# Kernel optimization log

Hardware: AMD Instinct MI355X
Metric: run time of the kernel (lower is better)

## Reference

```python
import jax, jax.numpy as jnp
import numpy as np

B, NAV, H, W = 16, 36, 120, 160
HID, AEMB, NF = 512, 32, 4

def _conv(x, w, b, stride, pad, dil, groups):
    y = jax.lax.conv_general_dilated(x, w, stride, pad, rhs_dilation=dil, feature_group_count=groups)
    return y + b[None, :, None, None]

def _avgpool(x, k, s):
    y = jax.lax.reduce_window(x, 0.0, jax.lax.add, (1, 1) + k, (1, 1) + s, 'VALID')
    return y / float(k[0] * k[1])

def _conv2_block(x, w1, b1, w2, b2):
    # conv2_1: k5 stride (5,7) dilation 10 -> avgpool 3/3 -> conv2_2: k3 stride 2 dilation (1,2) -> avgpool (3,9)/3
    y = _conv(x, w1, b1, (5, 7), ((0, 0), (0, 0)), (10, 10), 1)
    y = _avgpool(y, (3, 3), (3, 3))
    y = _conv(y, w2, b2, (2, 2), ((0, 0), (0, 0)), (1, 2), 1)
    y = _avgpool(y, (3, 9), (3, 3))
    return y[:, 0]  # [B,3,12]

def setup_inputs() -> dict:
    key = jax.random.key(0)
    ks = jax.random.split(key, 24)
    s = 0.02
    d = {}
    d['depth_feat_0'] = jax.random.normal(ks[0], (B, NAV, H, W), jnp.float32)
    d['depth_feat_1'] = jax.random.normal(ks[1], (B, NAV, H, W), jnp.float32)
    d['obj_detection_feat'] = jax.random.normal(ks[2], (B, NAV, H, W), jnp.float32)
    d['num_navigable_feat'] = jax.random.uniform(ks[3], (B, NAV), jnp.float32)
    d['pre_action_feat'] = jax.random.normal(ks[4], (B, AEMB), jnp.float32)
    d['h_0'] = jax.random.normal(ks[5], (B, HID), jnp.float32)
    d['c_0'] = jax.random.normal(ks[6], (B, HID), jnp.float32)
    d['weighted_ctx'] = jax.random.normal(ks[7], (B, HID), jnp.float32)
    d['navigable_index'] = jax.random.randint(ks[8], (B, 8), 0, NAV).astype(jnp.int32)
    # params
    d['conv1_w'] = jax.random.normal(ks[9], (NAV, 2, 5, 5), jnp.float32) * s
    d['conv1_b'] = jnp.zeros((NAV,), jnp.float32)
    d['dyn_filters'] = jax.random.normal(ks[10], (NF, NAV, 2, 5, 5), jnp.float32) * s
    d['dyn_w1'] = jax.random.normal(ks[11], (HID, HID // 4), jnp.float32) * s
    d['dyn_b1'] = jnp.zeros((HID // 4,), jnp.float32)
    d['dyn_w2'] = jax.random.normal(ks[12], (HID // 4, NF), jnp.float32) * s
    d['dyn_b2'] = jnp.zeros((NF,), jnp.float32)
    d['conv2_1_w'] = jax.random.normal(ks[13], (1, 1, 5, 5), jnp.float32) * s
    d['conv2_1_b'] = jnp.zeros((1,), jnp.float32)
    d['conv2_2_w'] = jax.random.normal(ks[14], (1, 1, 3, 3), jnp.float32) * s
    d['conv2_2_b'] = jnp.zeros((1,), jnp.float32)
    in_sz = HID + NAV + NF + AEMB  # 584
    d['lstm_w_ih'] = jax.random.normal(ks[15], (4 * HID, in_sz), jnp.float32) * s
    d['lstm_w_hh'] = jax.random.normal(ks[16], (4 * HID, HID), jnp.float32) * s
    d['lstm_b_ih'] = jnp.zeros((4 * HID,), jnp.float32)
    d['lstm_b_hh'] = jnp.zeros((4 * HID,), jnp.float32)
    return d

def reference(depth_feat_0, depth_feat_1, obj_detection_feat, num_navigable_feat, pre_action_feat, h_0, c_0, weighted_ctx, navigable_index, conv1_w, conv1_b, dyn_filters, dyn_w1, dyn_b1, dyn_w2, dyn_b2, conv2_1_w, conv2_1_b, conv2_2_w, conv2_2_b, lstm_w_ih, lstm_w_hh, lstm_b_ih, lstm_b_hh):
    Bv = depth_feat_0.shape[0]
    # interleave depth channels: [B,72,H,W] (replaces 36-iter python copy loop)
    mid1 = jnp.stack([depth_feat_0, depth_feat_1], axis=2).reshape(Bv, 2 * NAV, H, W)
    total_depth = _conv(mid1, conv1_w, conv1_b, (1, 1), ((2, 2), (2, 2)), (1, 1), NAV)  # [B,36,H,W]
    nav_attn = jax.nn.softmax(num_navigable_feat, axis=1)[:, :, None, None]
    mid2 = jnp.stack([total_depth * nav_attn, obj_detection_feat * nav_attn], axis=2).reshape(Bv, 2 * NAV, H, W)
    # dynamic conv: per-sample filter = attention-weighted mix of NF learned grouped filters
    filt_attn = jax.nn.softmax(jax.nn.relu(weighted_ctx @ dyn_w1 + dyn_b1) @ dyn_w2 + dyn_b2, axis=1)  # [B,4]
    kern = jnp.einsum('bf,fgikl->bgikl', filt_attn, dyn_filters).reshape(Bv * NAV, 2, 5, 5)
    dyn_out = jax.lax.conv_general_dilated(mid2.reshape(1, Bv * 2 * NAV, H, W), kern, (1, 1), ((2, 2), (2, 2)), feature_group_count=Bv * NAV).reshape(Bv, NAV, H, W)
    # panorama canvas assembly: tile i -> row block (2 - i//12), col i%12
    canvas = dyn_out.reshape(Bv, 3, 12, H, W)[:, ::-1].transpose(0, 1, 3, 2, 4).reshape(Bv, 1, 3 * H, 12 * W)
    v1 = _conv2_block(canvas, conv2_1_w, conv2_1_b, conv2_2_w, conv2_2_b)
    rolled = jnp.concatenate([canvas[..., -W:], canvas[..., :-W]], axis=-1)
    v2 = _conv2_block(rolled, conv2_1_w, conv2_1_b, conv2_2_w, conv2_2_b)
    v2 = jnp.concatenate([v2[:, :, 1:], v2[:, :, :1]], axis=-1)
    vf = ((v1 + v2) * 0.5)[:, ::-1].reshape(Bv, NAV)  # flip row dim then flatten
    vf = jax.nn.softmax(vf / 10.0, axis=1)  # self.softmax_temperature hardcoded to 10
    concat = jnp.concatenate([weighted_ctx, vf, filt_attn, pre_action_feat], axis=1)
    gates = concat @ lstm_w_ih.T + lstm_b_ih + h_0 @ lstm_w_hh.T + lstm_b_hh
    i, f, g, o = jnp.split(gates, 4, axis=1)
    c_1 = jax.nn.sigmoid(f) * c_0 + jax.nn.sigmoid(i) * jnp.tanh(g)
    h_1 = jax.nn.sigmoid(o) * jnp.tanh(c_1)
    mask = jnp.zeros((Bv, NAV + 1), jnp.float32).at[:, 0].set(1.0)
    mask = mask.at[jnp.arange(Bv)[:, None], navigable_index + 1].set(1.0)
    return (h_1, c_1, vf, mask)
```

## Files before the change

kernel.cpp:

```cpp
#include <hip/hip_runtime.h>
#include <math.h>

#define B_ 16
#define NAV_ 36
#define H_ 120
#define W_ 160
#define HID_ 512
#define PLANES (B_*NAV_)
#define PLANE_PX (H_*W_)
#define CANVAS_H 360
#define CANVAS_W 1920
#define CANVAS_PX (CANVAS_H*CANVAS_W)

#define OUT_H 12
#define IN_ROWS 20
#define TD_ROWS 16
#define OBJ_ROWS 16
#define ROWB 352
#define INCH (IN_ROWS*ROWB)
#define NSLOT (2*IN_ROWS*44 + OBJ_ROWS*44)
#define SPT 10

#define WS_NAV    0
#define WS_FATT   576
#define WS_KERN   640
#define WS_TD     29440
#define WS_CANVAS (WS_TD + PLANES*PLANE_PX)
#define WS_POOL1  (WS_CANVAS + B_*CANVAS_PX)
#define WS_VF     (WS_POOL1 + B_*2*19*89)

typedef unsigned int u32;
typedef _Float16 h2_t __attribute__((ext_vector_type(2)));
typedef float float4a __attribute__((ext_vector_type(4), aligned(4)));

__device__ __forceinline__ float sigmoidf_(float x) { return 1.f / (1.f + expf(-x)); }

__device__ __forceinline__ u32 pkh(float a, float b) {
    return __builtin_bit_cast(u32, __builtin_amdgcn_cvt_pkrtz(a, b));
}
__device__ __forceinline__ float dot2h(u32 a, u32 b, float c) {
#if __has_builtin(__builtin_amdgcn_fdot2)
    return __builtin_amdgcn_fdot2(__builtin_bit_cast(h2_t, a),
                                  __builtin_bit_cast(h2_t, b), c, false);
#else
    float r;
    asm("v_dot2_f32_f16 %0, %1, %2, %3" : "=v"(r) : "v"(a), "v"(b), "v"(c));
    return r;
#endif
}

__device__ __forceinline__ void conv8(const unsigned char* b0, const unsigned char* b1,
                                      const u32* ew, float* acc)
{
    #pragma unroll
    for (int ky = 0; ky < 5; ++ky) {
        const int off = ky*ROWB;
        int4 qa = *(const int4*)(b0 + off);
        int2 qb = *(const int2*)(b0 + off + 16);
        int4 ra = *(const int4*)(b1 + off);
        int2 rb = *(const int2*)(b1 + off + 16);
        u32 P[6] = {(u32)qa.x,(u32)qa.y,(u32)qa.z,(u32)qa.w,(u32)qb.x,(u32)qb.y};
        u32 Q[6] = {(u32)ra.x,(u32)ra.y,(u32)ra.z,(u32)ra.w,(u32)rb.x,(u32)rb.y};
        const u32 e0 = ew[ky*3+0], e1 = ew[ky*3+1], e2 = ew[ky*3+2];
        const u32 f0 = ew[15+ky*3+0], f1 = ew[15+ky*3+1], f2 = ew[15+ky*3+2];
        const u32 o0 = e0 << 16;
        const u32 o1 = __builtin_amdgcn_alignbit(e1, e0, 16);
        const u32 o2 = __builtin_amdgcn_alignbit(e2, e1, 16);
        const u32 g0 = f0 << 16;
        const u32 g1 = __builtin_amdgcn_alignbit(f1, f0, 16);
        const u32 g2 = __builtin_amdgcn_alignbit(f2, f1, 16);
        #pragma unroll
        for (int m = 0; m < 4; ++m) {
            acc[2*m]   = dot2h(e0, P[m], dot2h(e1, P[m+1], dot2h(e2, P[m+2], acc[2*m])));
            acc[2*m+1] = dot2h(o0, P[m], dot2h(o1, P[m+1], dot2h(o2, P[m+2], acc[2*m+1])));
            acc[2*m]   = dot2h(f0, Q[m], dot2h(f1, Q[m+1], dot2h(f2, Q[m+2], acc[2*m])));
            acc[2*m+1] = dot2h(g0, Q[m], dot2h(g1, Q[m+1], dot2h(g2, Q[m+2], acc[2*m+1])));
        }
    }
}

#define LOAD_EW(EW, SW)                                                        \
    {                                                                          \
        _Pragma("unroll")                                                      \
        for (int q = 0; q < 7; ++q) {                                          \
            int4 t_ = ((const int4*)(SW))[q];                                  \
            EW[4*q]=(u32)t_.x; EW[4*q+1]=(u32)t_.y; EW[4*q+2]=(u32)t_.z; EW[4*q+3]=(u32)t_.w; \
        }                                                                      \
        int2 t_ = ((const int2*)(SW))[14];                                     \
        EW[28]=(u32)t_.x; EW[29]=(u32)t_.y;                                    \
    }

__global__ __launch_bounds__(256)
void k_pre(const float* __restrict__ wctx, const float* __restrict__ dw1,
           const float* __restrict__ db1, const float* __restrict__ dw2,
           const float* __restrict__ db2, const float* __restrict__ dynf,
           const float* __restrict__ numnav, float* __restrict__ ws)
{
    const int tid = threadIdx.x;
    const int b = blockIdx.x;
    __shared__ float sh[128];
    __shared__ float sred[8];
    __shared__ float nv[36];
    __shared__ float nms[2];
    if (tid < 128) {
        float acc = db1[tid];
        for (int k = 0; k < HID_; ++k) acc += wctx[b*HID_ + k] * dw1[k*128 + tid];
        sh[tid] = fmaxf(acc, 0.f);
    }
    __syncthreads();
    if (tid < 4) {
        float acc = db2[tid];
        for (int j = 0; j < 128; ++j) acc += sh[j] * dw2[j*4 + tid];
        sred[tid] = acc;
    }
    __syncthreads();
    if (tid == 0) {
        float m = fmaxf(fmaxf(sred[0], sred[1]), fmaxf(sred[2], sred[3]));
        float e0 = expf(sred[0]-m), e1 = expf(sred[1]-m), e2 = expf(sred[2]-m), e3 = expf(sred[3]-m);
        float s = e0+e1+e2+e3;
        sred[4] = e0/s; sred[5] = e1/s; sred[6] = e2/s; sred[7] = e3/s;
        ws[WS_FATT + b*4+0] = sred[4]; ws[WS_FATT + b*4+1] = sred[5];
        ws[WS_FATT + b*4+2] = sred[6]; ws[WS_FATT + b*4+3] = sred[7];
    }
    __syncthreads();
    {
        const float fa0 = sred[4], fa1 = sred[5], fa2 = sred[6], fa3 = sred[7];
        for (int e = tid; e < 1800; e += 256) {
            float v = fa0*dynf[e] + fa1*dynf[1800+e] + fa2*dynf[3600+e] + fa3*dynf[5400+e];
            ws[WS_KERN + b*1800 + e] = v;
        }
    }
    if (tid < 36) nv[tid] = numnav[b*NAV_ + tid];
    __syncthreads();
    if (tid == 0) {
        float m = nv[0];
        for (int i = 1; i < 36; ++i) m = fmaxf(m, nv[i]);
        float s = 0.f;
        for (int i = 0; i < 36; ++i) s += expf(nv[i]-m);
        nms[0] = m; nms[1] = s;
    }
    __syncthreads();
    if (tid < 36) ws[WS_NAV + b*NAV_ + tid] = expf(nv[tid]-nms[0]) / nms[1];
}

__global__ __launch_bounds__(256)
void k_fused(const float* __restrict__ d0, const float* __restrict__ d1,
             const float* __restrict__ obj, const float* __restrict__ conv1_w,
             const float* __restrict__ conv1_b, float* __restrict__ ws)
{
    const int tid = threadIdx.x;
    const int half = blockIdx.x;
    const int plane = blockIdx.y;
    const int b = plane / NAV_;
    const int g = plane % NAV_;
    const int r0base = half * 5 * OUT_H;

    __shared__ __align__(16) unsigned char smem[2*INCH + OBJ_ROWS*ROWB + TD_ROWS*ROWB + 256];
    unsigned char* inL  = smem;
    unsigned char* objL = smem + 2*INCH;
    unsigned char* tdL  = objL + OBJ_ROWS*ROWB;
    u32* wts = (u32*)(tdL + TD_ROWS*ROWB);

    if (tid < 30) {
        const int ch = tid/15, ky = (tid%15)/3, k = tid%3;
        const float* wsrc = conv1_w + g*50 + ch*25 + ky*5;
        wts[tid] = pkh(wsrc[2*k], (k < 2) ? wsrc[2*k+1] : 0.f);
    } else if (tid >= 32 && tid < 62) {
        const int t2 = tid - 32;
        const int ch = t2/15, ky = (t2%15)/3, k = t2%3;
        const float* wsrc = ws + WS_KERN + plane*50 + ch*25 + ky*5;
        wts[tid] = pkh(wsrc[2*k], (k < 2) ? wsrc[2*k+1] : 0.f);
    } else if (tid == 62) ((float*)wts)[62] = conv1_b[g];
    else if (tid == 63)   ((float*)wts)[63] = ws[WS_NAV + plane];
    if (tid >= 64 && tid < 96) {
        const int t2 = tid - 64;
        const int rr = t2 >> 1;
        *(u32*)(tdL + rr*ROWB + ((t2 & 1) ? 324 : 0)) = 0;
    }

    const float* pd0 = d0 + (size_t)plane*PLANE_PX;
    const float* pd1 = d1 + (size_t)plane*PLANE_PX;
    const float* pob = obj + (size_t)plane*PLANE_PX;

    u32 meta[SPT];
    #pragma unroll
    for (int k = 0; k < SPT; ++k) {
        const int slot = tid + 256*k;
        u32 m = 0;
        if (slot < NSLOT) {
            int j, rr4, ss; u32 dst;
            if (slot < 2*IN_ROWS*44) {
                const int ch = slot / (IN_ROWS*44);
                const int rem = slot % (IN_ROWS*44);
                const int row = rem / 44;
                j = rem % 44; rr4 = row; ss = ch;
                dst = (u32)(ch*INCH + row*ROWB + j*8);
            } else {
                const int s2 = slot - 2*IN_ROWS*44;
                const int row = s2 / 44;
                j = s2 % 44; rr4 = row + 2; ss = 2;
                dst = (u32)(2*INCH + row*ROWB + j*8);
            }
            m = dst | ((u32)j << 15) | ((u32)rr4 << 21) | ((u32)ss << 26) | 0x80000000u;
        }
        meta[k] = m;
    }

    float4a pf[SPT];
    const float4a z4 = {0.f, 0.f, 0.f, 0.f};

    #define ISSUE(R0) {                                                        \
        _Pragma("unroll")                                                      \
        for (int k = 0; k < SPT; ++k) {                                        \
            float4a v = z4;                                                    \
            if (meta[k] & 0x80000000u) {                                       \
                const int j   = (int)((meta[k] >> 15) & 63u);                  \
                const int gr  = (R0) + (int)((meta[k] >> 21) & 31u) - 4;       \
                const int ss  = (int)((meta[k] >> 26) & 3u);                   \
                if ((unsigned)gr < (unsigned)H_ && j <= 40) {                  \
                    const float* src = (ss == 0) ? pd0 : ((ss == 1) ? pd1 : pob); \
                    const int co = (j == 0) ? 0 : ((j < 40) ? 4*j - 2 : 156);  \
                    v = *(const float4a*)(src + gr*W_ + co);                   \
                }                                                              \
            }                                                                  \
            pf[k] = v;                                                         \
        } }

    #define WRITEPF() {                                                        \
        _Pragma("unroll")                                                      \
        for (int k = 0; k < SPT; ++k) {                                        \
            if (meta[k] & 0x80000000u) {                                       \
                const int j = (int)((meta[k] >> 15) & 63u);                    \
                u32 lo = 0, hi = 0;                                            \
                if (j == 0)       { hi = pkh(pf[k].x, pf[k].y); }              \
                else if (j < 40)  { lo = pkh(pf[k].x, pf[k].y); hi = pkh(pf[k].z, pf[k].w); } \
                else if (j == 40) { lo = pkh(pf[k].z, pf[k].w); }              \
                *(int2*)(smem + (meta[k] & 0x7FFFu)) = make_int2((int)lo, (int)hi); \
            }                                                                  \
        } }

    ISSUE(r0base)
    WRITEPF()
    __syncthreads();

    for (int band = 0; band < 5; ++band) {
        const int r0 = r0base + band*OUT_H;
        if (band < 4) ISSUE(r0 + OUT_H)

        for (int t = tid; t < TD_ROWS*20; t += 256) {
            const int tr = t/20, s = t%20;
            const int gr = r0 - 2 + tr;
            u32* rowp = (u32*)(tdL + tr*ROWB);
            if ((unsigned)gr >= (unsigned)H_) {
                rowp[4*s+1] = 0;
                *(int2*)(rowp + 4*s + 2) = make_int2(0, 0);
                rowp[4*s+4] = 0;
                continue;
            }
            float acc[8];
            #pragma unroll
            for (int p = 0; p < 8; ++p) acc[p] = 0.f;
            u32 ew[30];
            LOAD_EW(ew, wts)
            conv8(inL + tr*ROWB + s*16, inL + INCH + tr*ROWB + s*16, ew, acc);
            const float bias = ((const float*)wts)[62];
            const u32 p0 = pkh(acc[0]+bias, acc[1]+bias);
            const u32 p1 = pkh(acc[2]+bias, acc[3]+bias);
            const u32 p2 = pkh(acc[4]+bias, acc[5]+bias);
            const u32 p3 = pkh(acc[6]+bias, acc[7]+bias);
            rowp[4*s+1] = p0;
            *(int2*)(rowp + 4*s + 2) = make_int2((int)p1, (int)p2);
            rowp[4*s+4] = p3;
        }
        __syncthreads();

        if (tid < OUT_H*20) {
            const int yr = tid/20, s = tid%20;
            float acc[8];
            #pragma unroll
            for (int p = 0; p < 8; ++p) acc[p] = 0.f;
            u32 ew[30];
            LOAD_EW(ew, wts + 32)
            conv8(tdL + yr*ROWB + s*16, objL + yr*ROWB + s*16, ew, acc);
            const float a = ((const float*)wts)[63];
            const int rowblk = 2 - g/12;
            const int colblk = g % 12;
            float* cbase = ws + WS_CANVAS + (size_t)b*CANVAS_PX
                         + (size_t)(rowblk*H_ + r0 + yr)*CANVAS_W + colblk*W_ + s*8;
            *(float4*)cbase     = make_float4(a*acc[0], a*acc[1], a*acc[2], a*acc[3]);
            *(float4*)(cbase+4) = make_float4(a*acc[4], a*acc[5], a*acc[6], a*acc[7]);
        }
        __syncthreads();

        if (band < 4) {
            WRITEPF()
            __syncthreads();
        }
    }
}

__global__ __launch_bounds__(256)
void k_conv2a(const float* __restrict__ w21p, const float* __restrict__ b21p,
              float* __restrict__ ws)
{
    const int blk = blockIdx.x;
    const int a = blk % 19;
    const int bv = blk / 19;
    const int ver = bv & 1;
    const int b = bv >> 1;
    const int coloff = ver ? (CANVAS_W - W_) : 0;

    __shared__ float s1[3*267];
    __shared__ float swt[25];
    if (threadIdx.x < 25) swt[threadIdx.x] = w21p[threadIdx.x];
    __syncthreads();
    const float b21 = b21p[0];
    const float* cv = ws + WS_CANVAS + (size_t)b*CANVAS_PX;

    for (int px = threadIdx.x; px < 3*267; px += 256) {
        const int row = px / 267;
        const int v = px % 267;
        const int u = 3*a + row;
        float acc = b21;
        #pragma unroll
        for (int ky = 0; ky < 5; ++ky) {
            const float* rp = cv + (5*u + 10*ky)*CANVAS_W;
            #pragma unroll
            for (int kx = 0; kx < 5; ++kx) {
                int c = 7*v + 10*kx + coloff;
                if (c >= CANVAS_W) c -= CANVAS_W;
                acc += swt[ky*5+kx] * rp[c];
            }
        }
        s1[px] = acc;
    }
    __syncthreads();
    if (threadIdx.x < 89) {
        const int bb = threadIdx.x;
        float s = 0.f;
        #pragma unroll
        for (int i = 0; i < 3; ++i)
            #pragma unroll
            for (int j = 0; j < 3; ++j)
                s += s1[i*267 + 3*bb + j];
        ws[WS_POOL1 + blk*89 + bb] = s * (1.f/9.f);
    }
}

__global__ __launch_bounds__(256)
void k_conv2b(const float* __restrict__ w22p, const float* __restrict__ b22p,
              const int* __restrict__ navidx, float* __restrict__ ws,
              float* __restrict__ out)
{
    const int b = blockIdx.x;
    __shared__ float p[2*19*89];
    __shared__ float s2[2*9*43];
    __shared__ float svf[36];
    __shared__ float sms[2];
    __shared__ float swt[9];

    for (int i = threadIdx.x; i < 2*19*89; i += 256)
        p[i] = ws[WS_POOL1 + (b*2)*19*89 + i];
    if (threadIdx.x < 9) swt[threadIdx.x] = w22p[threadIdx.x];
    const float b22 = b22p[0];
    __syncthreads();

    for (int t = threadIdx.x; t < 2*9*43; t += 256) {
        const int ver = t / 387;
        const int r = t % 387;
        const int pp = r / 43;
        const int q = r % 43;
        float acc = b22;
        #pragma unroll
        for (int i = 0; i < 3; ++i)
            #pragma unroll
            for (int j = 0; j < 3; ++j)
                acc += swt[i*3+j] * p[(ver*19 + (2*pp+i))*89 + 2*q + 2*j];
        s2[ver*387 + pp*43 + q] = acc;
    }
    __syncthreads();

    if (threadIdx.x < 36) {
        const int gg = threadIdx.x;
        const int io = 2 - gg/12;
        const int j  = gg % 12;
        const int j2 = (j + 1) % 12;
        float s = 0.f;
        #pragma unroll
        for (int ii = 0; ii < 3; ++ii)
            #pragma unroll
            for (int jj = 0; jj < 9; ++jj)
                s += s2[(3*io+ii)*43 + 3*j + jj] + s2[387 + (3*io+ii)*43 + 3*j2 + jj];
        svf[gg] = s * (0.5f/27.f);
    }
    __syncthreads();
    if (threadIdx.x == 0) {
        float m = svf[0];
        for (int i = 1; i < 36; ++i) m = fmaxf(m, svf[i]);
        float s = 0.f;
        for (int i = 0; i < 36; ++i) s += expf((svf[i]-m)*0.1f);
        sms[0] = m; sms[1] = s;
    }
    __syncthreads();
    if (threadIdx.x < 36) {
        const float v = expf((svf[threadIdx.x]-sms[0])*0.1f) / sms[1];
        ws[WS_VF + b*36 + threadIdx.x] = v;
        out[16384 + b*36 + threadIdx.x] = v;
    }
    if (threadIdx.x < 37) {
        const int j = threadIdx.x;
        float v = (j == 0) ? 1.f : 0.f;
        #pragma unroll
        for (int t = 0; t < 8; ++t)
            if (navidx[b*8+t] + 1 == j) v = 1.f;
        out[16960 + b*37 + j] = v;
    }
}

#define CT_STRIDE 20
__global__ __launch_bounds__(256)
void k_lstm(const float* __restrict__ wctx, const float* __restrict__ pre_action,
            const float* __restrict__ h0, const float* __restrict__ c0,
            const float* __restrict__ w_ih, const float* __restrict__ w_hh,
            const float* __restrict__ b_ih, const float* __restrict__ b_hh,
            const float* __restrict__ ws, float* __restrict__ out)
{
    __shared__ float cT[1096*CT_STRIDE];
    __shared__ float red[8*32*16];
    __shared__ float gatev[8][16];
    const int tid = threadIdx.x;

    for (int idx = tid; idx < 1096*16; idx += 256) {
        const int k = idx >> 4;
        const int bb = idx & 15;
        float v;
        if (k < 512)       v = wctx[bb*512 + k];
        else if (k < 548)  v = ws[WS_VF + bb*36 + (k-512)];
        else if (k < 552)  v = ws[WS_FATT + bb*4 + (k-548)];
        else if (k < 584)  v = pre_action[bb*32 + (k-552)];
        else               v = h0[bb*512 + (k-584)];
        cT[k*CT_STRIDE + bb] = v;
    }
    __syncthreads();

    const int rl = tid >> 5;
    const int lane = tid & 31;
    const int u0 = blockIdx.x*2;
    const int ul = rl & 1;
    const int gate = rl >> 1;
    const int r = u0 + ul + gate*512;

    float acc[16];
    #pragma unroll
    for (int i = 0; i < 16; ++i) acc[i] = 0.f;

    const float* wih_r = w_ih + (size_t)r*584;
    for (int k = lane; k < 584; k += 32) {
        const float wv = wih_r[k];
        const float* cp = cT + k*CT_STRIDE;
        #pragma unroll
        for (int i = 0; i < 16; ++i) acc[i] += wv*cp[i];
    }
    const float* whh_r = w_hh + (size_t)r*512;
    for (int k = lane; k < 512; k += 32) {
        const float wv = whh_r[k];
        const float* cp = cT + (584+k)*CT_STRIDE;
        #pragma unroll
        for (int i = 0; i < 16; ++i) acc[i] += wv*cp[i];
    }
    float* rp = red + (rl*32 + lane)*16;
    #pragma unroll
    for (int i = 0; i < 16; ++i) rp[i] = acc[i];
    __syncthreads();

    if (tid < 128) {
        const int rr = tid >> 4;
        const int bb = tid & 15;
        const int rrow = u0 + (rr & 1) + (rr >> 1)*512;
        float s = b_ih[rrow] + b_hh[rrow];
        for (int l = 0; l < 32; ++l) s += red[(rr*32 + l)*16 + bb];
        gatev[rr][bb] = s;
    }
    __syncthreads();

    if (tid < 32) {
        const int ul2 = tid >> 4;
        const int bb = tid & 15;
        const int u = u0 + ul2;
        const float gi = gatev[0+ul2][bb];
        const float gf = gatev[2+ul2][bb];
        const float gg = gatev[4+ul2][bb];
        const float go = gatev[6+ul2][bb];
        const float c1 = sigmoidf_(gf)*c0[bb*512+u] + sigmoidf_(gi)*tanhf(gg);
        const float h1 = sigmoidf_(go)*tanhf(c1);
        out[bb*512 + u] = h1;
        out[8192 + bb*512 + u] = c1;
    }
}

extern "C" void kernel_launch(void* const* d_in, const int* in_sizes, int n_in,
                              void* d_out, int out_size, void* d_ws, size_t ws_size,
                              hipStream_t stream)
{
    const float* d0        = (const float*)d_in[0];
    const float* d1        = (const float*)d_in[1];
    const float* obj       = (const float*)d_in[2];
    const float* numnav    = (const float*)d_in[3];
    const float* preact    = (const float*)d_in[4];
    const float* h0        = (const float*)d_in[5];
    const float* c0        = (const float*)d_in[6];
    const float* wctx      = (const float*)d_in[7];
    const int*   navidx    = (const int*)d_in[8];
    const float* conv1_w   = (const float*)d_in[9];
    const float* conv1_b   = (const float*)d_in[10];
    const float* dynf      = (const float*)d_in[11];
    const float* dw1       = (const float*)d_in[12];
    const float* db1       = (const float*)d_in[13];
    const float* dw2       = (const float*)d_in[14];
    const float* db2       = (const float*)d_in[15];
    const float* w21       = (const float*)d_in[16];
    const float* b21       = (const float*)d_in[17];
    const float* w22       = (const float*)d_in[18];
    const float* b22       = (const float*)d_in[19];
    const float* wih       = (const float*)d_in[20];
    const float* whh       = (const float*)d_in[21];
    const float* bih       = (const float*)d_in[22];
    const float* bhh       = (const float*)d_in[23];
    float* ws  = (float*)d_ws;
    float* out = (float*)d_out;

    dim3 blk(256);
    k_pre   <<<dim3(16),      blk, 0, stream>>>(wctx, dw1, db1, dw2, db2, dynf, numnav, ws);
    k_fused <<<dim3(2, 576),  blk, 0, stream>>>(d0, d1, obj, conv1_w, conv1_b, ws);
    k_conv2a<<<dim3(608),     blk, 0, stream>>>(w21, b21, ws);
    k_conv2b<<<dim3(16),      blk, 0, stream>>>(w22, b22, navidx, ws, out);
    k_lstm  <<<dim3(256),     blk, 0, stream>>>(wctx, preact, h0, c0, wih, whh,
                                                bih, bhh, ws, out);
}
```

Measured before the change: 146.6 us.

## Split fused conv into more row-band blocks and precompute odd-shifted weights in LDS

The fused conv kernel now runs 5 blocks per plane, each doing 2 bands of 12 output rows, instead of 2 blocks doing 5 bands each. This raises grid parallelism and shortens each block's serial pipeline, at the cost of more halo rows reloaded and more per-block setup. The odd-offset packed half weights are computed once into shared memory rather than realigned in registers per thread, and the conv reads weights straight from LDS instead of loading a 30-entry register array. The LSTM staging loop's index order is also changed so global reads are contiguous along k.

```diff
diff --git a/kernel.cpp b/kernel.cpp
--- a/kernel.cpp
+++ b/kernel.cpp
@@ -13,6 +13,7 @@
 #define CANVAS_PX (CANVAS_H*CANVAS_W)
 
 #define OUT_H 12
+#define NBAND 2
 #define IN_ROWS 20
 #define TD_ROWS 16
 #define OBJ_ROWS 16
@@ -50,7 +51,8 @@
 }
 
 __device__ __forceinline__ void conv8(const unsigned char* b0, const unsigned char* b1,
-                                      const u32* ew, float* acc)
+                                      const u32* __restrict__ ew,
+                                      const u32* __restrict__ ow, float* acc)
 {
     #pragma unroll
     for (int ky = 0; ky < 5; ++ky) {
@@ -62,13 +64,9 @@
         u32 P[6] = {(u32)qa.x,(u32)qa.y,(u32)qa.z,(u32)qa.w,(u32)qb.x,(u32)qb.y};
         u32 Q[6] = {(u32)ra.x,(u32)ra.y,(u32)ra.z,(u32)ra.w,(u32)rb.x,(u32)rb.y};
         const u32 e0 = ew[ky*3+0], e1 = ew[ky*3+1], e2 = ew[ky*3+2];
+        const u32 o0 = ow[ky*3+0], o1 = ow[ky*3+1], o2 = ow[ky*3+2];
         const u32 f0 = ew[15+ky*3+0], f1 = ew[15+ky*3+1], f2 = ew[15+ky*3+2];
-        const u32 o0 = e0 << 16;
-        const u32 o1 = __builtin_amdgcn_alignbit(e1, e0, 16);
-        const u32 o2 = __builtin_amdgcn_alignbit(e2, e1, 16);
-        const u32 g0 = f0 << 16;
-        const u32 g1 = __builtin_amdgcn_alignbit(f1, f0, 16);
-        const u32 g2 = __builtin_amdgcn_alignbit(f2, f1, 16);
+        const u32 g0 = ow[15+ky*3+0], g1 = ow[15+ky*3+1], g2 = ow[15+ky*3+2];
         #pragma unroll
         for (int m = 0; m < 4; ++m) {
             acc[2*m]   = dot2h(e0, P[m], dot2h(e1, P[m+1], dot2h(e2, P[m+2], acc[2*m])));
@@ -78,17 +76,6 @@
         }
     }
 }
-
-#define LOAD_EW(EW, SW)                                                        \
-    {                                                                          \
-        _Pragma("unroll")                                                      \
-        for (int q = 0; q < 7; ++q) {                                          \
-            int4 t_ = ((const int4*)(SW))[q];                                  \
-            EW[4*q]=(u32)t_.x; EW[4*q+1]=(u32)t_.y; EW[4*q+2]=(u32)t_.z; EW[4*q+3]=(u32)t_.w; \
-        }                                                                      \
-        int2 t_ = ((const int2*)(SW))[14];                                     \
-        EW[28]=(u32)t_.x; EW[29]=(u32)t_.y;                                    \
-    }
 
 __global__ __launch_bounds__(256)
 void k_pre(const float* __restrict__ wctx, const float* __restrict__ dw1,
@@ -149,13 +136,12 @@
              const float* __restrict__ conv1_b, float* __restrict__ ws)
 {
     const int tid = threadIdx.x;
-    const int half = blockIdx.x;
     const int plane = blockIdx.y;
     const int b = plane / NAV_;
     const int g = plane % NAV_;
-    const int r0base = half * 5 * OUT_H;
-
-    __shared__ __align__(16) unsigned char smem[2*INCH + OBJ_ROWS*ROWB + TD_ROWS*ROWB + 256];
+    const int r0base = blockIdx.x * (NBAND*OUT_H);
+
+    __shared__ __align__(16) unsigned char smem[2*INCH + OBJ_ROWS*ROWB + TD_ROWS*ROWB + 512];
     unsigned char* inL  = smem;
     unsigned char* objL = smem + 2*INCH;
     unsigned char* tdL  = objL + OBJ_ROWS*ROWB;
@@ -169,9 +155,9 @@
         const int t2 = tid - 32;
         const int ch = t2/15, ky = (t2%15)/3, k = t2%3;
         const float* wsrc = ws + WS_KERN + plane*50 + ch*25 + ky*5;
-        wts[tid] = pkh(wsrc[2*k], (k < 2) ? wsrc[2*k+1] : 0.f);
-    } else if (tid == 62) ((float*)wts)[62] = conv1_b[g];
-    else if (tid == 63)   ((float*)wts)[63] = ws[WS_NAV + plane];
+        wts[64 + t2] = pkh(wsrc[2*k], (k < 2) ? wsrc[2*k+1] : 0.f);
+    } else if (tid == 62) ((float*)wts)[126] = conv1_b[g];
+    else if (tid == 63)   ((float*)wts)[127] = ws[WS_NAV + plane];
     if (tid >= 64 && tid < 96) {
         const int t2 = tid - 64;
         const int rr = t2 >> 1;
@@ -243,9 +229,22 @@
     WRITEPF()
     __syncthreads();
 
-    for (int band = 0; band < 5; ++band) {
+    if (tid < 60) {
+        const int conv = tid / 30;
+        const int i = tid % 30;
+        const u32* evn = wts + conv*64;
+        u32* odd = wts + conv*64 + 32;
+        const int b3 = (i/3)*3, k = i%3;
+        u32 v;
+        if (k == 0) v = evn[b3] << 16;
+        else        v = __builtin_amdgcn_alignbit(evn[b3+k], evn[b3+k-1], 16);
+        odd[i] = v;
+    }
+    __syncthreads();
+
+    for (int band = 0; band < NBAND; ++band) {
         const int r0 = r0base + band*OUT_H;
-        if (band < 4) ISSUE(r0 + OUT_H)
+        if (band < NBAND-1) ISSUE(r0 + OUT_H)
 
         for (int t = tid; t < TD_ROWS*20; t += 256) {
             const int tr = t/20, s = t%20;
@@ -260,10 +259,9 @@
             float acc[8];
             #pragma unroll
             for (int p = 0; p < 8; ++p) acc[p] = 0.f;
-            u32 ew[30];
-            LOAD_EW(ew, wts)
-            conv8(inL + tr*ROWB + s*16, inL + INCH + tr*ROWB + s*16, ew, acc);
-            const float bias = ((const float*)wts)[62];
+            conv8(inL + tr*ROWB + s*16, inL + INCH + tr*ROWB + s*16,
+                  wts, wts + 32, acc);
+            const float bias = ((const float*)wts)[126];
             const u32 p0 = pkh(acc[0]+bias, acc[1]+bias);
             const u32 p1 = pkh(acc[2]+bias, acc[3]+bias);
             const u32 p2 = pkh(acc[4]+bias, acc[5]+bias);
@@ -279,10 +277,9 @@
             float acc[8];
             #pragma unroll
             for (int p = 0; p < 8; ++p) acc[p] = 0.f;
-            u32 ew[30];
-            LOAD_EW(ew, wts + 32)
-            conv8(tdL + yr*ROWB + s*16, objL + yr*ROWB + s*16, ew, acc);
-            const float a = ((const float*)wts)[63];
+            conv8(tdL + yr*ROWB + s*16, objL + yr*ROWB + s*16,
+                  wts + 64, wts + 96, acc);
+            const float a = ((const float*)wts)[127];
             const int rowblk = 2 - g/12;
             const int colblk = g % 12;
             float* cbase = ws + WS_CANVAS + (size_t)b*CANVAS_PX
@@ -292,7 +289,7 @@
         }
         __syncthreads();
 
-        if (band < 4) {
+        if (band < NBAND-1) {
             WRITEPF()
             __syncthreads();
         }
@@ -431,8 +428,8 @@
     const int tid = threadIdx.x;
 
     for (int idx = tid; idx < 1096*16; idx += 256) {
-        const int k = idx >> 4;
-        const int bb = idx & 15;
+        const int bb = idx / 1096;
+        const int k = idx - bb*1096;
         float v;
         if (k < 512)       v = wctx[bb*512 + k];
         else if (k < 548)  v = ws[WS_VF + bb*36 + (k-512)];
@@ -531,7 +528,7 @@
 
     dim3 blk(256);
     k_pre   <<<dim3(16),      blk, 0, stream>>>(wctx, dw1, db1, dw2, db2, dynf, numnav, ws);
-    k_fused <<<dim3(2, 576),  blk, 0, stream>>>(d0, d1, obj, conv1_w, conv1_b, ws);
+    k_fused <<<dim3(5, 576),  blk, 0, stream>>>(d0, d1, obj, conv1_w, conv1_b, ws);
     k_conv2a<<<dim3(608),     blk, 0, stream>>>(w21, b21, ws);
     k_conv2b<<<dim3(16),      blk, 0, stream>>>(w22, b22, navidx, ws, out);
     k_lstm  <<<dim3(256),     blk, 0, stream>>>(wctx, preact, h0, c0, wih, whh,
```

Result: slower. 166.2 us (+13.3%).

## Store canvas as fp16 and stage needed rows in LDS for conv2_1

Applied to the files above, without the earlier changes.

The fused dynamic-conv kernel now writes the panorama canvas as packed fp16 instead of fp32, halving canvas write traffic. k_conv2a is relaunched as a 19x16 grid where each block loads only the 11 canvas rows it needs into shared memory. Both the normal and the rolled version are computed from that one copy, so reads are shared between them. The LSTM staging loop index order is also changed to make global reads contiguous. The cost is fp16 rounding of the canvas values and a large LDS footprint per block.

```diff
diff --git a/kernel.cpp b/kernel.cpp
--- a/kernel.cpp
+++ b/kernel.cpp
@@ -30,6 +30,7 @@
 #define WS_VF     (WS_POOL1 + B_*2*19*89)
 
 typedef unsigned int u32;
+typedef unsigned short u16;
 typedef _Float16 h2_t __attribute__((ext_vector_type(2)));
 typedef float float4a __attribute__((ext_vector_type(4), aligned(4)));
 
@@ -37,6 +38,10 @@
 
 __device__ __forceinline__ u32 pkh(float a, float b) {
     return __builtin_bit_cast(u32, __builtin_amdgcn_cvt_pkrtz(a, b));
+}
+__device__ __forceinline__ float h2f(u16 h) {
+    _Float16 v = __builtin_bit_cast(_Float16, h);
+    return (float)v;
 }
 __device__ __forceinline__ float dot2h(u32 a, u32 b, float c) {
 #if __has_builtin(__builtin_amdgcn_fdot2)
@@ -285,10 +290,13 @@
             const float a = ((const float*)wts)[63];
             const int rowblk = 2 - g/12;
             const int colblk = g % 12;
-            float* cbase = ws + WS_CANVAS + (size_t)b*CANVAS_PX
-                         + (size_t)(rowblk*H_ + r0 + yr)*CANVAS_W + colblk*W_ + s*8;
-            *(float4*)cbase     = make_float4(a*acc[0], a*acc[1], a*acc[2], a*acc[3]);
-            *(float4*)(cbase+4) = make_float4(a*acc[4], a*acc[5], a*acc[6], a*acc[7]);
+            u16* cb = (u16*)(ws + WS_CANVAS) + (size_t)b*CANVAS_PX
+                    + (size_t)(rowblk*H_ + r0 + yr)*CANVAS_W + colblk*W_ + s*8;
+            const u32 q0 = pkh(a*acc[0], a*acc[1]);
+            const u32 q1 = pkh(a*acc[2], a*acc[3]);
+            const u32 q2 = pkh(a*acc[4], a*acc[5]);
+            const u32 q3 = pkh(a*acc[6], a*acc[7]);
+            *(int4*)cb = make_int4((int)q0, (int)q1, (int)q2, (int)q3);
         }
         __syncthreads();
 
@@ -303,47 +311,56 @@
 void k_conv2a(const float* __restrict__ w21p, const float* __restrict__ b21p,
               float* __restrict__ ws)
 {
-    const int blk = blockIdx.x;
-    const int a = blk % 19;
-    const int bv = blk / 19;
-    const int ver = bv & 1;
-    const int b = bv >> 1;
-    const int coloff = ver ? (CANVAS_W - W_) : 0;
-
-    __shared__ float s1[3*267];
+    const int a = blockIdx.x;
+    const int b = blockIdx.y;
+    const int tid = threadIdx.x;
+
+    __shared__ __align__(16) u16 cvh[11*CANVAS_W];
+    __shared__ float s1[2*801];
     __shared__ float swt[25];
-    if (threadIdx.x < 25) swt[threadIdx.x] = w21p[threadIdx.x];
-    __syncthreads();
+    if (tid < 25) swt[tid] = w21p[tid];
     const float b21 = b21p[0];
-    const float* cv = ws + WS_CANVAS + (size_t)b*CANVAS_PX;
-
-    for (int px = threadIdx.x; px < 3*267; px += 256) {
+
+    const u16* cvsrc = (const u16*)(ws + WS_CANVAS) + (size_t)b*CANVAS_PX;
+    for (int i = tid; i < 11*240; i += 256) {
+        const int k = i / 240;
+        const int c8 = i % 240;
+        *(int4*)&cvh[k*CANVAS_W + c8*8] =
+            *(const int4*)(cvsrc + (size_t)(15*a + 5*k)*CANVAS_W + c8*8);
+    }
+    __syncthreads();
+
+    for (int t = tid; t < 2*801; t += 256) {
+        const int ver = t / 801;
+        const int px = t % 801;
         const int row = px / 267;
         const int v = px % 267;
-        const int u = 3*a + row;
+        const int coloff = ver ? (CANVAS_W - W_) : 0;
         float acc = b21;
         #pragma unroll
         for (int ky = 0; ky < 5; ++ky) {
-            const float* rp = cv + (5*u + 10*ky)*CANVAS_W;
+            const u16* rp = &cvh[(row + 2*ky)*CANVAS_W];
             #pragma unroll
             for (int kx = 0; kx < 5; ++kx) {
                 int c = 7*v + 10*kx + coloff;
                 if (c >= CANVAS_W) c -= CANVAS_W;
-                acc += swt[ky*5+kx] * rp[c];
+                acc += swt[ky*5+kx] * h2f(rp[c]);
             }
         }
-        s1[px] = acc;
-    }
-    __syncthreads();
-    if (threadIdx.x < 89) {
-        const int bb = threadIdx.x;
+        s1[ver*801 + px] = acc;
+    }
+    __syncthreads();
+
+    if (tid < 2*89) {
+        const int ver = tid / 89;
+        const int bb = tid % 89;
         float s = 0.f;
         #pragma unroll
         for (int i = 0; i < 3; ++i)
             #pragma unroll
             for (int j = 0; j < 3; ++j)
-                s += s1[i*267 + 3*bb + j];
-        ws[WS_POOL1 + blk*89 + bb] = s * (1.f/9.f);
+                s += s1[ver*801 + i*267 + 3*bb + j];
+        ws[WS_POOL1 + ((b*2 + ver)*19 + a)*89 + bb] = s * (1.f/9.f);
     }
 }
 
@@ -431,8 +448,8 @@
     const int tid = threadIdx.x;
 
     for (int idx = tid; idx < 1096*16; idx += 256) {
-        const int k = idx >> 4;
-        const int bb = idx & 15;
+        const int bb = idx / 1096;
+        const int k = idx - bb*1096;
         float v;
         if (k < 512)       v = wctx[bb*512 + k];
         else if (k < 548)  v = ws[WS_VF + bb*36 + (k-512)];
@@ -532,7 +549,7 @@
     dim3 blk(256);
     k_pre   <<<dim3(16),      blk, 0, stream>>>(wctx, dw1, db1, dw2, db2, dynf, numnav, ws);
     k_fused <<<dim3(2, 576),  blk, 0, stream>>>(d0, d1, obj, conv1_w, conv1_b, ws);
-    k_conv2a<<<dim3(608),     blk, 0, stream>>>(w21, b21, ws);
+    k_conv2a<<<dim3(19, 16),  blk, 0, stream>>>(w21, b21, ws);
     k_conv2b<<<dim3(16),      blk, 0, stream>>>(w22, b22, navidx, ws, out);
     k_lstm  <<<dim3(256),     blk, 0, stream>>>(wctx, preact, h0, c0, wih, whh,
                                                 bih, bhh, ws, out);
```

Measured after the change: 137.5 us. -6.2%, faster.
